# Kernel optimization log

Hardware: AMD Instinct MI355X
Metric: run time of the kernel (lower is better)

Reference implementation:

```python
import jax, jax.numpy as jnp
import numpy as np

N_EMBED = 1024
HEAD_SIZE = 64
BLOCK_SIZE = 2048

def setup_inputs() -> dict:
    key = jax.random.key(0)
    kx, kq, kk, kv = jax.random.split(key, 4)
    scale = N_EMBED ** -0.5
    x = jax.random.normal(kx, (8, 2048, N_EMBED), dtype=jnp.float32)
    # nn.Linear weights stored as [out, in]; we keep [in, out] for x @ W
    Wq = jax.random.normal(kq, (N_EMBED, HEAD_SIZE), dtype=jnp.float32) * scale
    Wk = jax.random.normal(kk, (N_EMBED, HEAD_SIZE), dtype=jnp.float32) * scale
    Wv = jax.random.normal(kv, (N_EMBED, HEAD_SIZE), dtype=jnp.float32) * scale
    return {"x": x, "Wq": Wq, "Wk": Wk, "Wv": Wv}

def reference(x, Wq, Wk, Wv):
    B, T, C = x.shape
    q = x @ Wq  # [B,T,H]
    k = x @ Wk
    v = x @ Wv
    # NOTE: original scales by C**-0.5 (n_embed), not head_size**-0.5
    wei = jnp.einsum('bth,bsh->bts', q, k) * (C ** -0.5)  # [B,T,T]
    causal = jnp.tril(jnp.ones((T, T), dtype=bool))
    wei = jnp.where(causal, wei, -jnp.inf)
    wei = jax.nn.softmax(wei, axis=-1)
    out = jnp.einsum('bts,bsh->bth', wei, v)  # [B,T,H]
    return out
```

## Files before the change

### kernel.cpp

```cpp
#include <hip/hip_runtime.h>

#define B_ 8
#define T_ 2048
#define C_ 1024
#define H_ 64

typedef __attribute__((ext_vector_type(8))) short short8;
typedef __attribute__((ext_vector_type(4))) float floatx4;
typedef __attribute__((ext_vector_type(4))) int intx4;

static __device__ __forceinline__ unsigned short f2bf(float f) {
  unsigned int u = __builtin_bit_cast(unsigned int, f);
  u += 0x7FFFu + ((u >> 16) & 1u);
  return (unsigned short)(u >> 16);
}
static __device__ __forceinline__ float bf2f(unsigned short u) {
  return __builtin_bit_cast(float, ((unsigned int)u) << 16);
}
static __device__ __forceinline__ unsigned int fbits(float f) {
  return __builtin_bit_cast(unsigned int, f);
}

typedef const __attribute__((address_space(1))) unsigned int* gp1_t;
typedef __attribute__((address_space(3))) unsigned int* lp3_t;
static __device__ __forceinline__ void gl_lds16(const void* g, void* l) {
  __builtin_amdgcn_global_load_lds((gp1_t)g, (lp3_t)l, 16, 0, 0);
}

__global__ __launch_bounds__(256) void conv_w(const float* __restrict__ wq,
    const float* __restrict__ wk, const float* __restrict__ wv,
    unsigned short* __restrict__ wt) {
  int idx = blockIdx.x * 256 + threadIdx.x;
  int mat = idx >> 14;
  int e = idx & 16383;
  int kk = e >> 4, c0 = (e & 15) * 4;
  const float* src = (mat == 0) ? wq : (mat == 1) ? wk : wv;
  float scale = (mat == 0) ? 0.03125f * 1.44269504088896340736f : 1.0f;
  float4 v = *(const float4*)&src[kk * H_ + c0];
  wt[(size_t)(mat * 64 + c0 + 0) * C_ + kk] = f2bf(v.x * scale);
  wt[(size_t)(mat * 64 + c0 + 1) * C_ + kk] = f2bf(v.y * scale);
  wt[(size_t)(mat * 64 + c0 + 2) * C_ + kk] = f2bf(v.z * scale);
  wt[(size_t)(mat * 64 + c0 + 3) * C_ + kk] = f2bf(v.w * scale);
}

__global__ __launch_bounds__(256) void qkv_proj(
    const float* __restrict__ x, const unsigned short* __restrict__ wt,
    unsigned short* __restrict__ qo, unsigned short* __restrict__ ko,
    unsigned short* __restrict__ vT) {
  __shared__ float XL[2][4096];
  __shared__ unsigned short WL[2][12288];
  int tid = threadIdx.x;
  int wave = tid >> 6, lane = tid & 63;
  int lane4 = lane & 15, quad = lane >> 4;
  int m0 = blockIdx.x * 64;

  floatx4 acc[4][3];
#pragma unroll
  for (int mt = 0; mt < 4; ++mt)
#pragma unroll
    for (int nt = 0; nt < 3; ++nt) acc[mt][nt] = (floatx4)0.0f;

#pragma unroll
  for (int j = 0; j < 4; ++j) {
    int p = (wave * 4 + j) * 64 + lane;
    int r = p >> 4, pc = p & 15;
    int cl = (pc & 8) | ((pc ^ (r & 7)) & 7);
    gl_lds16(&x[(size_t)(m0 + r) * C_ + cl * 4], &XL[0][(wave * 4 + j) * 256]);
  }
#pragma unroll
  for (int j = 0; j < 6; ++j) {
    int p = (wave * 6 + j) * 64 + lane;
    int r = p >> 3, pc = p & 7;
    int cl = pc ^ (r & 7);
    gl_lds16(&wt[(size_t)r * C_ + cl * 8], &WL[0][(wave * 6 + j) * 512]);
  }
  __syncthreads();

  for (int kt = 0; kt < 16; ++kt) {
    int buf = kt & 1;
    if (kt < 15) {
      int k0 = (kt + 1) * 64;
#pragma unroll
      for (int j = 0; j < 4; ++j) {
        int p = (wave * 4 + j) * 64 + lane;
        int r = p >> 4, pc = p & 15;
        int cl = (pc & 8) | ((pc ^ (r & 7)) & 7);
        gl_lds16(&x[(size_t)(m0 + r) * C_ + k0 + cl * 4], &XL[buf ^ 1][(wave * 4 + j) * 256]);
      }
#pragma unroll
      for (int j = 0; j < 6; ++j) {
        int p = (wave * 6 + j) * 64 + lane;
        int r = p >> 3, pc = p & 7;
        int cl = pc ^ (r & 7);
        gl_lds16(&wt[(size_t)r * C_ + k0 + cl * 8], &WL[buf ^ 1][(wave * 6 + j) * 512]);
      }
    }

#pragma unroll
    for (int ks = 0; ks < 2; ++ks) {
      short8 a[4];
#pragma unroll
      for (int mt = 0; mt < 4; ++mt) {
        int r = mt * 16 + lane4;
        int cl0 = ks * 8 + quad * 2;
        int pc0 = (cl0 & 8) | ((cl0 ^ (r & 7)) & 7);
        int pc1 = ((cl0 + 1) & 8) | (((cl0 + 1) ^ (r & 7)) & 7);
        float4 f0 = *(const float4*)&XL[buf][r * 64 + pc0 * 4];
        float4 f1 = *(const float4*)&XL[buf][r * 64 + pc1 * 4];
        intx4 pk;
        pk[0] = (int)__builtin_amdgcn_perm(fbits(f0.y), fbits(f0.x), 0x07060302u);
        pk[1] = (int)__builtin_amdgcn_perm(fbits(f0.w), fbits(f0.z), 0x07060302u);
        pk[2] = (int)__builtin_amdgcn_perm(fbits(f1.y), fbits(f1.x), 0x07060302u);
        pk[3] = (int)__builtin_amdgcn_perm(fbits(f1.w), fbits(f1.z), 0x07060302u);
        a[mt] = __builtin_bit_cast(short8, pk);
      }
      short8 b[3];
#pragma unroll
      for (int nt = 0; nt < 3; ++nt) {
        int r = (wave * 3 + nt) * 16 + lane4;
        int cl = ks * 4 + quad;
        int pc = cl ^ (r & 7);
        b[nt] = *(const short8*)&WL[buf][r * 64 + pc * 8];
      }
#pragma unroll
      for (int mt = 0; mt < 4; ++mt)
#pragma unroll
        for (int nt = 0; nt < 3; ++nt)
          acc[mt][nt] = __builtin_amdgcn_mfma_f32_16x16x32_bf16(a[mt], b[nt], acc[mt][nt], 0, 0, 0);
    }
    __syncthreads();
  }

  unsigned short* VTB = (unsigned short*)&XL[0][0];
#pragma unroll
  for (int mt = 0; mt < 4; ++mt)
#pragma unroll
    for (int nt = 0; nt < 3; ++nt) {
      int n = (wave * 3 + nt) * 16 + lane4;
#pragma unroll
      for (int rr = 0; rr < 4; ++rr) {
        unsigned short val = f2bf(acc[mt][nt][rr]);
        int lrow = mt * 16 + quad * 4 + rr;
        if (n < 64)       qo[(size_t)(m0 + lrow) * H_ + n] = val;
        else if (n < 128) ko[(size_t)(m0 + lrow) * H_ + n - 64] = val;
        else              VTB[(n - 128) * 80 + lrow] = val;
      }
    }
  __syncthreads();
  {
    int h = tid >> 2, ch = tid & 3;
    int batch = m0 >> 11, t0 = m0 & 2047;
    uint4 v0 = *(const uint4*)&VTB[h * 80 + ch * 16];
    uint4 v1 = *(const uint4*)&VTB[h * 80 + ch * 16 + 8];
    unsigned short* dst = &vT[(size_t)(batch * 64 + h) * T_ + t0 + ch * 16];
    *(uint4*)dst = v0;
    *(uint4*)&dst[8] = v1;
  }
}

__global__ __launch_bounds__(256, 2) void attn(
    const unsigned short* __restrict__ qi, const unsigned short* __restrict__ ki,
    const unsigned short* __restrict__ vT, unsigned short* __restrict__ Op,
    float* __restrict__ lsum) {
  __shared__ unsigned short KL[2][64][72];
  __shared__ unsigned short VL[2][64][72];
  __shared__ float PL[4][16][84];

  int tid = threadIdx.x;
  int wave = tid >> 6, lane = tid & 63;
  int lane4 = lane & 15, quad = lane >> 4;
  int qt = blockIdx.x, b = blockIdx.y, split = blockIdx.z;
  int qb = qt * 64;
  int base = b * T_;

  int ntile = qt + 1;
  int sBeg = (split * ntile) >> 2;
  int sEnd = ((split + 1) * ntile) >> 2;

  short8 aq[2];
#pragma unroll
  for (int ks = 0; ks < 2; ++ks)
    aq[ks] = *(const short8*)&qi[(size_t)(base + qb + wave * 16 + lane4) * H_ + ks * 32 + quad * 8];

  float lrow[4];
  floatx4 o[4];
#pragma unroll
  for (int r = 0; r < 4; ++r) lrow[r] = 0.0f;
#pragma unroll
  for (int nt = 0; nt < 4; ++nt) o[nt] = (floatx4)0.0f;

  int r0 = tid >> 3, c8 = (tid & 7) * 8;
  const unsigned short* vt0 = &vT[((size_t)b * H_ + r0) * T_];
  const unsigned short* vt1 = &vT[((size_t)b * H_ + r0 + 32) * T_];

  if (sBeg < sEnd) {
    uint4 k0v, k1v, v0v, v1v;
    {
      int s0 = sBeg * 64;
      k0v = *(const uint4*)&ki[(size_t)(base + s0 + r0) * H_ + c8];
      k1v = *(const uint4*)&ki[(size_t)(base + s0 + r0 + 32) * H_ + c8];
      v0v = *(const uint4*)&vt0[s0 + c8];
      v1v = *(const uint4*)&vt1[s0 + c8];
    }
    *(uint4*)&KL[0][r0][c8] = k0v;
    *(uint4*)&KL[0][r0 + 32][c8] = k1v;
    *(uint4*)&VL[0][r0][c8] = v0v;
    *(uint4*)&VL[0][r0 + 32][c8] = v1v;
    __syncthreads();

    for (int st = sBeg; st < sEnd; ++st) {
      int bufi = (st - sBeg) & 1;
      bool hasnext = (st + 1 < sEnd);
      if (hasnext) {
        int s0 = (st + 1) * 64;
        k0v = *(const uint4*)&ki[(size_t)(base + s0 + r0) * H_ + c8];
        k1v = *(const uint4*)&ki[(size_t)(base + s0 + r0 + 32) * H_ + c8];
        v0v = *(const uint4*)&vt0[s0 + c8];
        v1v = *(const uint4*)&vt1[s0 + c8];
      }

      floatx4 sacc[4];
#pragma unroll
      for (int ct = 0; ct < 4; ++ct) sacc[ct] = (floatx4)0.0f;
#pragma unroll
      for (int ks = 0; ks < 2; ++ks)
#pragma unroll
        for (int ct = 0; ct < 4; ++ct) {
          short8 bk = *(const short8*)&KL[bufi][ct * 16 + lane4][ks * 32 + quad * 8];
          sacc[ct] = __builtin_amdgcn_mfma_f32_16x16x32_bf16(aq[ks], bk, sacc[ct], 0, 0, 0);
        }

      if (st == qt) {
#pragma unroll
        for (int ct = 0; ct < 4; ++ct)
#pragma unroll
          for (int r = 0; r < 4; ++r) {
            int srow = wave * 16 + quad * 4 + r;
            int scol = ct * 16 + lane4;
            if (scol > srow) sacc[ct][r] = -3.0e38f;
          }
      }

#pragma unroll
      for (int ct = 0; ct < 4; ++ct)
#pragma unroll
        for (int r = 0; r < 4; ++r) {
          float p = exp2f(sacc[ct][r] - 8.0f);
          lrow[r] += p;
          PL[wave][quad * 4 + r][ct * 16 + lane4] = p;
        }

#pragma unroll
      for (int ks = 0; ks < 2; ++ks) {
        float4 pa0 = *(const float4*)&PL[wave][lane4][ks * 32 + quad * 8];
        float4 pa1 = *(const float4*)&PL[wave][lane4][ks * 32 + quad * 8 + 4];
        short8 pa;
        pa[0] = (short)f2bf(pa0.x); pa[1] = (short)f2bf(pa0.y);
        pa[2] = (short)f2bf(pa0.z); pa[3] = (short)f2bf(pa0.w);
        pa[4] = (short)f2bf(pa1.x); pa[5] = (short)f2bf(pa1.y);
        pa[6] = (short)f2bf(pa1.z); pa[7] = (short)f2bf(pa1.w);
#pragma unroll
        for (int nt = 0; nt < 4; ++nt) {
          short8 bv = *(const short8*)&VL[bufi][nt * 16 + lane4][ks * 32 + quad * 8];
          o[nt] = __builtin_amdgcn_mfma_f32_16x16x32_bf16(pa, bv, o[nt], 0, 0, 0);
        }
      }

      if (hasnext) {
        int nb = bufi ^ 1;
        *(uint4*)&KL[nb][r0][c8] = k0v;
        *(uint4*)&KL[nb][r0 + 32][c8] = k1v;
        *(uint4*)&VL[nb][r0][c8] = v0v;
        *(uint4*)&VL[nb][r0 + 32][c8] = v1v;
      }
      __syncthreads();
    }
  }

#pragma unroll
  for (int off = 1; off < 16; off <<= 1)
#pragma unroll
    for (int r = 0; r < 4; ++r) lrow[r] += __shfl_xor(lrow[r], off);

  size_t pbase = (((size_t)split * 8 + b) * 32 + qt) * 64;
#pragma unroll
  for (int r = 0; r < 4; ++r) {
    int row = wave * 16 + quad * 4 + r;
#pragma unroll
    for (int nt = 0; nt < 4; ++nt)
      Op[(pbase + row) * 64 + nt * 16 + lane4] = f2bf(o[nt][r]);
    if (lane4 == 0) lsum[pbase + row] = lrow[r];
  }
}

__global__ __launch_bounds__(256) void merge_splits(
    const unsigned short* __restrict__ Op, const float* __restrict__ lsum,
    float* __restrict__ out) {
  int idx = blockIdx.x * 256 + threadIdx.x;
  int row = idx >> 4;
  int h4 = (idx & 15) * 4;
  int b = row >> 11, t = row & 2047;
  int qt = t >> 6, r = t & 63;
  float O0 = 0.f, O1 = 0.f, O2 = 0.f, O3 = 0.f, l = 0.f;
#pragma unroll
  for (int s = 0; s < 4; ++s) {
    size_t p = (((size_t)s * 8 + b) * 32 + qt) * 64 + r;
    l += lsum[p];
    ushort4 ov = *(const ushort4*)&Op[p * 64 + h4];
    O0 += bf2f(ov.x); O1 += bf2f(ov.y); O2 += bf2f(ov.z); O3 += bf2f(ov.w);
  }
  float inv = 1.0f / l;
  float4 res = make_float4(O0 * inv, O1 * inv, O2 * inv, O3 * inv);
  *(float4*)&out[(size_t)row * H_ + h4] = res;
}

extern "C" void kernel_launch(void* const* d_in, const int* in_sizes, int n_in,
                              void* d_out, int out_size, void* d_ws, size_t ws_size,
                              hipStream_t stream) {
  const float* x  = (const float*)d_in[0];
  const float* wq = (const float*)d_in[1];
  const float* wk = (const float*)d_in[2];
  const float* wv = (const float*)d_in[3];
  float* out = (float*)d_out;

  char* ws = (char*)d_ws;
  unsigned short* wt = (unsigned short*)ws;
  unsigned short* qb = (unsigned short*)(ws + 393216);
  unsigned short* kb = (unsigned short*)(ws + 2490368);
  unsigned short* vt = (unsigned short*)(ws + 4587520);
  unsigned short* Op = (unsigned short*)(ws + 6684672);
  float*          ls = (float*)(ws + 15073280);

  conv_w<<<192, 256, 0, stream>>>(wq, wk, wv, wt);
  qkv_proj<<<256, 256, 0, stream>>>(x, wt, qb, kb, vt);
  attn<<<dim3(32, 8, 4), 256, 0, stream>>>(qb, kb, vt, Op, ls);
  merge_splits<<<1024, 256, 0, stream>>>(Op, ls, out);
}
```

Baseline: 149.2 us.

## Halve projection tile rows, async-load attention K/V into swizzled LDS, store P as bf16

The QKV projection now uses 32-row tiles, which doubles the grid to 512 blocks for more parallelism and halves the x staging buffer. The attention kernel replaces its register-staged K/V prefetch with direct global-to-LDS loads into XOR-swizzled unpadded buffers. It also converts P to bf16 before writing it to LDS, so reads are a single short8 with no per-element conversion. The occupancy hint of 2 on attn is removed. Smaller projection tiles re-read the weight tile more often, and dropping the occupancy hint may change register allocation.

```diff
diff --git a/kernel.cpp b/kernel.cpp
--- a/kernel.cpp
+++ b/kernel.cpp
@@ -47,25 +47,25 @@
     const float* __restrict__ x, const unsigned short* __restrict__ wt,
     unsigned short* __restrict__ qo, unsigned short* __restrict__ ko,
     unsigned short* __restrict__ vT) {
-  __shared__ float XL[2][4096];
+  __shared__ float XL[2][2048];
   __shared__ unsigned short WL[2][12288];
   int tid = threadIdx.x;
   int wave = tid >> 6, lane = tid & 63;
   int lane4 = lane & 15, quad = lane >> 4;
-  int m0 = blockIdx.x * 64;
-
-  floatx4 acc[4][3];
-#pragma unroll
-  for (int mt = 0; mt < 4; ++mt)
+  int m0 = blockIdx.x * 32;
+
+  floatx4 acc[2][3];
+#pragma unroll
+  for (int mt = 0; mt < 2; ++mt)
 #pragma unroll
     for (int nt = 0; nt < 3; ++nt) acc[mt][nt] = (floatx4)0.0f;
 
 #pragma unroll
-  for (int j = 0; j < 4; ++j) {
-    int p = (wave * 4 + j) * 64 + lane;
+  for (int j = 0; j < 2; ++j) {
+    int p = (wave * 2 + j) * 64 + lane;
     int r = p >> 4, pc = p & 15;
     int cl = (pc & 8) | ((pc ^ (r & 7)) & 7);
-    gl_lds16(&x[(size_t)(m0 + r) * C_ + cl * 4], &XL[0][(wave * 4 + j) * 256]);
+    gl_lds16(&x[(size_t)(m0 + r) * C_ + cl * 4], &XL[0][(wave * 2 + j) * 256]);
   }
 #pragma unroll
   for (int j = 0; j < 6; ++j) {
@@ -81,11 +81,11 @@
     if (kt < 15) {
       int k0 = (kt + 1) * 64;
 #pragma unroll
-      for (int j = 0; j < 4; ++j) {
-        int p = (wave * 4 + j) * 64 + lane;
+      for (int j = 0; j < 2; ++j) {
+        int p = (wave * 2 + j) * 64 + lane;
         int r = p >> 4, pc = p & 15;
         int cl = (pc & 8) | ((pc ^ (r & 7)) & 7);
-        gl_lds16(&x[(size_t)(m0 + r) * C_ + k0 + cl * 4], &XL[buf ^ 1][(wave * 4 + j) * 256]);
+        gl_lds16(&x[(size_t)(m0 + r) * C_ + k0 + cl * 4], &XL[buf ^ 1][(wave * 2 + j) * 256]);
       }
 #pragma unroll
       for (int j = 0; j < 6; ++j) {
@@ -98,9 +98,9 @@
 
 #pragma unroll
     for (int ks = 0; ks < 2; ++ks) {
-      short8 a[4];
-#pragma unroll
-      for (int mt = 0; mt < 4; ++mt) {
+      short8 a[2];
+#pragma unroll
+      for (int mt = 0; mt < 2; ++mt) {
         int r = mt * 16 + lane4;
         int cl0 = ks * 8 + quad * 2;
         int pc0 = (cl0 & 8) | ((cl0 ^ (r & 7)) & 7);
@@ -123,7 +123,7 @@
         b[nt] = *(const short8*)&WL[buf][r * 64 + pc * 8];
       }
 #pragma unroll
-      for (int mt = 0; mt < 4; ++mt)
+      for (int mt = 0; mt < 2; ++mt)
 #pragma unroll
         for (int nt = 0; nt < 3; ++nt)
           acc[mt][nt] = __builtin_amdgcn_mfma_f32_16x16x32_bf16(a[mt], b[nt], acc[mt][nt], 0, 0, 0);
@@ -133,38 +133,35 @@
 
   unsigned short* VTB = (unsigned short*)&XL[0][0];
 #pragma unroll
-  for (int mt = 0; mt < 4; ++mt)
+  for (int mt = 0; mt < 2; ++mt)
 #pragma unroll
     for (int nt = 0; nt < 3; ++nt) {
-      int n = (wave * 3 + nt) * 16 + lane4;
+      int n = wave * 48 + nt * 16 + lane4;
 #pragma unroll
       for (int rr = 0; rr < 4; ++rr) {
         unsigned short val = f2bf(acc[mt][nt][rr]);
         int lrow = mt * 16 + quad * 4 + rr;
         if (n < 64)       qo[(size_t)(m0 + lrow) * H_ + n] = val;
         else if (n < 128) ko[(size_t)(m0 + lrow) * H_ + n - 64] = val;
-        else              VTB[(n - 128) * 80 + lrow] = val;
+        else              VTB[(n - 128) * 40 + lrow] = val;
       }
     }
   __syncthreads();
   {
     int h = tid >> 2, ch = tid & 3;
     int batch = m0 >> 11, t0 = m0 & 2047;
-    uint4 v0 = *(const uint4*)&VTB[h * 80 + ch * 16];
-    uint4 v1 = *(const uint4*)&VTB[h * 80 + ch * 16 + 8];
-    unsigned short* dst = &vT[(size_t)(batch * 64 + h) * T_ + t0 + ch * 16];
-    *(uint4*)dst = v0;
-    *(uint4*)&dst[8] = v1;
-  }
-}
-
-__global__ __launch_bounds__(256, 2) void attn(
+    uint4 v0 = *(const uint4*)&VTB[h * 40 + ch * 8];
+    *(uint4*)&vT[(size_t)(batch * 64 + h) * T_ + t0 + ch * 8] = v0;
+  }
+}
+
+__global__ __launch_bounds__(256) void attn(
     const unsigned short* __restrict__ qi, const unsigned short* __restrict__ ki,
     const unsigned short* __restrict__ vT, unsigned short* __restrict__ Op,
     float* __restrict__ lsum) {
-  __shared__ unsigned short KL[2][64][72];
-  __shared__ unsigned short VL[2][64][72];
-  __shared__ float PL[4][16][84];
+  __shared__ unsigned short KL[2][4096];
+  __shared__ unsigned short VL[2][4096];
+  __shared__ unsigned short PL[4][16][72];
 
   int tid = threadIdx.x;
   int wave = tid >> 6, lane = tid & 63;
@@ -189,23 +186,19 @@
 #pragma unroll
   for (int nt = 0; nt < 4; ++nt) o[nt] = (floatx4)0.0f;
 
-  int r0 = tid >> 3, c8 = (tid & 7) * 8;
-  const unsigned short* vt0 = &vT[((size_t)b * H_ + r0) * T_];
-  const unsigned short* vt1 = &vT[((size_t)b * H_ + r0 + 32) * T_];
+  int srow = lane >> 3, sc = lane & 7;
 
   if (sBeg < sEnd) {
-    uint4 k0v, k1v, v0v, v1v;
     {
       int s0 = sBeg * 64;
-      k0v = *(const uint4*)&ki[(size_t)(base + s0 + r0) * H_ + c8];
-      k1v = *(const uint4*)&ki[(size_t)(base + s0 + r0 + 32) * H_ + c8];
-      v0v = *(const uint4*)&vt0[s0 + c8];
-      v1v = *(const uint4*)&vt1[s0 + c8];
-    }
-    *(uint4*)&KL[0][r0][c8] = k0v;
-    *(uint4*)&KL[0][r0 + 32][c8] = k1v;
-    *(uint4*)&VL[0][r0][c8] = v0v;
-    *(uint4*)&VL[0][r0 + 32][c8] = v1v;
+#pragma unroll
+      for (int j = 0; j < 2; ++j) {
+        int r = (wave * 2 + j) * 8 + srow;
+        int cl = sc ^ (r & 7);
+        gl_lds16(&ki[(size_t)(base + s0 + r) * H_ + cl * 8], &KL[0][(wave * 2 + j) * 512]);
+        gl_lds16(&vT[((size_t)b * H_ + r) * T_ + s0 + cl * 8], &VL[0][(wave * 2 + j) * 512]);
+      }
+    }
     __syncthreads();
 
     for (int st = sBeg; st < sEnd; ++st) {
@@ -213,10 +206,14 @@
       bool hasnext = (st + 1 < sEnd);
       if (hasnext) {
         int s0 = (st + 1) * 64;
-        k0v = *(const uint4*)&ki[(size_t)(base + s0 + r0) * H_ + c8];
-        k1v = *(const uint4*)&ki[(size_t)(base + s0 + r0 + 32) * H_ + c8];
-        v0v = *(const uint4*)&vt0[s0 + c8];
-        v1v = *(const uint4*)&vt1[s0 + c8];
+        int nb = bufi ^ 1;
+#pragma unroll
+        for (int j = 0; j < 2; ++j) {
+          int r = (wave * 2 + j) * 8 + srow;
+          int cl = sc ^ (r & 7);
+          gl_lds16(&ki[(size_t)(base + s0 + r) * H_ + cl * 8], &KL[nb][(wave * 2 + j) * 512]);
+          gl_lds16(&vT[((size_t)b * H_ + r) * T_ + s0 + cl * 8], &VL[nb][(wave * 2 + j) * 512]);
+        }
       }
 
       floatx4 sacc[4];
@@ -226,7 +223,9 @@
       for (int ks = 0; ks < 2; ++ks)
 #pragma unroll
         for (int ct = 0; ct < 4; ++ct) {
-          short8 bk = *(const short8*)&KL[bufi][ct * 16 + lane4][ks * 32 + quad * 8];
+          int r = ct * 16 + lane4;
+          int pc = (ks * 4 + quad) ^ (r & 7);
+          short8 bk = *(const short8*)&KL[bufi][r * 64 + pc * 8];
           sacc[ct] = __builtin_amdgcn_mfma_f32_16x16x32_bf16(aq[ks], bk, sacc[ct], 0, 0, 0);
         }
 
@@ -235,9 +234,9 @@
         for (int ct = 0; ct < 4; ++ct)
 #pragma unroll
           for (int r = 0; r < 4; ++r) {
-            int srow = wave * 16 + quad * 4 + r;
+            int qrow = wave * 16 + quad * 4 + r;
             int scol = ct * 16 + lane4;
-            if (scol > srow) sacc[ct][r] = -3.0e38f;
+            if (scol > qrow) sacc[ct][r] = -3.0e38f;
           }
       }
 
@@ -247,31 +246,19 @@
         for (int r = 0; r < 4; ++r) {
           float p = exp2f(sacc[ct][r] - 8.0f);
           lrow[r] += p;
-          PL[wave][quad * 4 + r][ct * 16 + lane4] = p;
+          PL[wave][quad * 4 + r][ct * 16 + lane4] = f2bf(p);
         }
 
 #pragma unroll
       for (int ks = 0; ks < 2; ++ks) {
-        float4 pa0 = *(const float4*)&PL[wave][lane4][ks * 32 + quad * 8];
-        float4 pa1 = *(const float4*)&PL[wave][lane4][ks * 32 + quad * 8 + 4];
-        short8 pa;
-        pa[0] = (short)f2bf(pa0.x); pa[1] = (short)f2bf(pa0.y);
-        pa[2] = (short)f2bf(pa0.z); pa[3] = (short)f2bf(pa0.w);
-        pa[4] = (short)f2bf(pa1.x); pa[5] = (short)f2bf(pa1.y);
-        pa[6] = (short)f2bf(pa1.z); pa[7] = (short)f2bf(pa1.w);
+        short8 pa = *(const short8*)&PL[wave][lane4][ks * 32 + quad * 8];
 #pragma unroll
         for (int nt = 0; nt < 4; ++nt) {
-          short8 bv = *(const short8*)&VL[bufi][nt * 16 + lane4][ks * 32 + quad * 8];
+          int r = nt * 16 + lane4;
+          int pc = (ks * 4 + quad) ^ (r & 7);
+          short8 bv = *(const short8*)&VL[bufi][r * 64 + pc * 8];
           o[nt] = __builtin_amdgcn_mfma_f32_16x16x32_bf16(pa, bv, o[nt], 0, 0, 0);
         }
-      }
-
-      if (hasnext) {
-        int nb = bufi ^ 1;
-        *(uint4*)&KL[nb][r0][c8] = k0v;
-        *(uint4*)&KL[nb][r0 + 32][c8] = k1v;
-        *(uint4*)&VL[nb][r0][c8] = v0v;
-        *(uint4*)&VL[nb][r0 + 32][c8] = v1v;
       }
       __syncthreads();
     }
@@ -332,7 +319,7 @@
   float*          ls = (float*)(ws + 15073280);
 
   conv_w<<<192, 256, 0, stream>>>(wq, wk, wv, wt);
-  qkv_proj<<<256, 256, 0, stream>>>(x, wt, qb, kb, vt);
+  qkv_proj<<<512, 256, 0, stream>>>(x, wt, qb, kb, vt);
   attn<<<dim3(32, 8, 4), 256, 0, stream>>>(qb, kb, vt, Op, ls);
   merge_splits<<<1024, 256, 0, stream>>>(Op, ls, out);
 }
```

Result: faster. 145.9 us (-2.2%).
